# Optimization experiments

Hardware: AMD Instinct MI355X
Metric: run time of the kernel (lower is better)

## Reference

```python
import jax, jax.numpy as jnp
import numpy as np

B, H_, W_, C, HEADS, WS, SR = 4, 56, 56, 256, 8, 3, 4
HD = C // HEADS
N = H_ * W_
LL = WS * WS
PH, PW = H_ // SR, W_ // SR
PL = PH * PW
K_TAB = 2048


def _unfold3(x, H, W):
    # x: (B, C, H, W) -> (B, C, 9, H*W); matches torch nn.Unfold(kernel_size=3, padding=1)
    xp = jnp.pad(x, ((0, 0), (0, 0), (1, 1), (1, 1)))
    pats = jnp.stack([xp[:, :, i:i + H, j:j + W] for i in range(3) for j in range(3)], axis=2)
    return pats.reshape(x.shape[0], x.shape[1], 9, H * W)


def _l2n(x):
    # torch F.normalize(dim=-1) with eps=1e-12
    return x / jnp.maximum(jnp.linalg.norm(x, axis=-1, keepdims=True), 1e-12)


def setup_inputs() -> dict:
    key = jax.random.key(0)
    ks = jax.random.split(key, 24)
    x = jax.random.normal(ks[0], (B, N, C), jnp.float32)
    # padding mask from unfold of ones image (True where window element falls outside)
    ones = np.zeros((H_ + 2, W_ + 2), np.float32)
    ones[1:-1, 1:-1] = 1.0
    pats = np.stack([ones[i:i + H_, j:j + W_] for i in range(3) for j in range(3)], 0).reshape(9, N)
    padding_mask = jnp.asarray((pats == 0).T)  # (N, 9) bool
    local_valid = LL - padding_mask.sum(-1)
    seq_length_scale = jnp.log(local_valid.astype(jnp.float32) + PL)[:, None]  # (N,1)
    relative_pos_index = jax.random.randint(ks[1], (N * PL,), 0, K_TAB)
    relative_coords_table = jax.random.uniform(ks[2], (K_TAB, 2), jnp.float32, -1.0, 1.0)
    w = lambda k, shape: jax.random.normal(k, shape, jnp.float32) * 0.02
    inp = dict(
        x=x, H=H_, W=W_,
        relative_pos_index=relative_pos_index,
        relative_coords_table=relative_coords_table,
        seq_length_scale=seq_length_scale,
        padding_mask=padding_mask,
        q_w=w(ks[3], (C, C)), q_b=jnp.zeros((C,), jnp.float32),
        kv_w=w(ks[4], (2 * C, C)), kv_b=jnp.zeros((2 * C,), jnp.float32),
        sr_w=w(ks[5], (C, C)), sr_b=jnp.zeros((C,), jnp.float32),
        norm_g=jnp.ones((C,), jnp.float32), norm_b=jnp.zeros((C,), jnp.float32),
        cpb1_w=w(ks[6], (512, 2)), cpb1_b=jnp.zeros((512,), jnp.float32),
        cpb2_w=w(ks[7], (HEADS, 512)), cpb2_b=jnp.zeros((HEADS,), jnp.float32),
        temperature=jnp.log(jnp.exp(jnp.ones((HEADS, 1, 1), jnp.float32) / 0.24) - 1.0),
        query_embedding=w(ks[8], (HEADS, 1, HD)),
        rel_pos_bias_local=jax.random.normal(ks[9], (HEADS, LL), jnp.float32) * 0.0004,
        learnable_tokens=w(ks[10], (HEADS, HD, LL)),
        learnable_bias=jnp.zeros((HEADS, 1, LL), jnp.float32),
        proj_w=w(ks[11], (C, C)), proj_b=jnp.zeros((C,), jnp.float32),
    )
    return inp


def reference(x, H, W, relative_pos_index, relative_coords_table, seq_length_scale,
              padding_mask, q_w, q_b, kv_w, kv_b, sr_w, sr_b, norm_g, norm_b,
              cpb1_w, cpb1_b, cpb2_w, cpb2_b, temperature, query_embedding,
              rel_pos_bias_local, learnable_tokens, learnable_bias, proj_w, proj_b):
    Bsz, n, Cd = x.shape
    h, hd, ll = HEADS, HD, LL
    pH, pW = H // SR, W // SR
    pL = pH * pW
    # ----- queries -----
    q = (x @ q_w.T + q_b).reshape(Bsz, n, h, hd).transpose(0, 2, 1, 3)  # (B,h,N,d)
    q_norm = _l2n(q)
    q_scaled = (q_norm + query_embedding) * jax.nn.softplus(temperature) * seq_length_scale
    # ----- local branch: unfolded window KV -----
    kv = x @ kv_w.T + kv_b  # (B,N,2C)
    k_loc, v_loc = jnp.split(kv, 2, axis=-1)
    k_loc = _l2n(k_loc.reshape(Bsz, n, h, hd)).reshape(Bsz, n, Cd)
    kv_img = jnp.concatenate([k_loc, v_loc], -1).transpose(0, 2, 1).reshape(Bsz, 2 * Cd, H, W)
    pats = _unfold3(kv_img, H, W).reshape(Bsz, 2 * h, hd, ll, n).transpose(0, 1, 4, 2, 3)  # (B,2h,N,d,ll)
    k_local, v_local = jnp.split(pats, 2, axis=1)
    attn_local = jnp.einsum('bhnd,bhndl->bhnl', q_scaled, k_local) + rel_pos_bias_local[:, None, :]
    attn_local = jnp.where(padding_mask, -jnp.inf, attn_local)
    # ----- global branch: 1x1 conv -> GELU -> avg pool -> LN -> KV -----
    x_img = x.transpose(0, 2, 1).reshape(Bsz, Cd, H, W)
    x_sr = jax.nn.gelu(jnp.einsum('oc,bchw->bohw', sr_w, x_img) + sr_b[None, :, None, None], approximate=False)
    x_pool = x_sr.reshape(Bsz, Cd, pH, SR, pW, SR).mean(axis=(3, 5)).reshape(Bsz, Cd, pL).transpose(0, 2, 1)
    mu = x_pool.mean(-1, keepdims=True)
    var = x_pool.var(-1, keepdims=True)
    x_pool = (x_pool - mu) / jnp.sqrt(var + 1e-5) * norm_g + norm_b
    kvp = (x_pool @ kv_w.T + kv_b).reshape(Bsz, pL, 2 * h, hd).transpose(0, 2, 1, 3)
    k_pool, v_pool = jnp.split(kvp, 2, axis=1)  # each (B,h,pL,d)
    # CPB-MLP relative position bias (interpolate is identity since test==trained resolution)
    tab = jax.nn.relu(relative_coords_table @ cpb1_w.T + cpb1_b) @ cpb2_w.T + cpb2_b  # (K,h)
    pool_bias = tab.T[:, relative_pos_index].reshape(h, n, pL)
    attn_pool = jnp.einsum('bhnd,bhmd->bhnm', q_scaled, _l2n(k_pool)) + pool_bias
    # ----- joint softmax over [local | pool] -----
    attn = jax.nn.softmax(jnp.concatenate([attn_local, attn_pool], axis=-1), axis=-1)
    a_loc, a_pool = attn[..., :ll], attn[..., ll:]
    w_loc = jnp.einsum('bhnd,hdl->bhnl', q_norm, learnable_tokens) + learnable_bias + a_loc
    x_local = jnp.einsum('bhnl,bhndl->bhnd', w_loc, v_local)
    x_glob = jnp.einsum('bhnm,bhmd->bhnd', a_pool, v_pool)
    out = (x_local + x_glob).transpose(0, 2, 1, 3).reshape(Bsz, n, Cd)
    return out @ proj_w.T + proj_b
```

## Files before the change

kernel.cpp:

```cpp
#include <hip/hip_runtime.h>
#include <hip/hip_bf16.h>
#include <math.h>

#define Bn   4
#define Hh   56
#define Wn   56
#define Cn   256
#define NHn  8
#define HDn  32
#define Nn   3136
#define LLn  9
#define PLn  196
#define PWn  14
#define KTABn 2048
#define Mrows 12544
#define MP   224

#define XCNT   3211264
#define QWOFF  XCNT
#define KVWOFF (QWOFF + 65536)
#define SRWOFF (KVWOFF + 131072)
#define PWOFF  (SRWOFF + 65536)
#define TOTCVT (PWOFF + 65536)

typedef __attribute__((ext_vector_type(8))) short short8v;
typedef __attribute__((ext_vector_type(4))) float float4v;

__device__ __forceinline__ unsigned short f2b(float f) {
  __hip_bfloat16 h = __float2bfloat16(f);
  return *(unsigned short*)&h;
}
__device__ __forceinline__ float b2f(unsigned short u) {
  union { unsigned int i; float f; } x; x.i = ((unsigned int)u) << 16; return x.f;
}
__device__ __forceinline__ void u4_to8f(uint4 u, float* o) {
  o[0]=b2f((unsigned short)(u.x&0xffff)); o[1]=b2f((unsigned short)(u.x>>16));
  o[2]=b2f((unsigned short)(u.y&0xffff)); o[3]=b2f((unsigned short)(u.y>>16));
  o[4]=b2f((unsigned short)(u.z&0xffff)); o[5]=b2f((unsigned short)(u.z>>16));
  o[6]=b2f((unsigned short)(u.w&0xffff)); o[7]=b2f((unsigned short)(u.w>>16));
}

__launch_bounds__(256)
__global__ void cvt5(const float* __restrict__ x, const float* __restrict__ qw,
                     const float* __restrict__ kvw, const float* __restrict__ srw,
                     const float* __restrict__ pw, unsigned short* __restrict__ dst)
{
  const int i = (blockIdx.x * 256 + threadIdx.x) * 4;
  const float* src; int off;
  if      (i < XCNT)   { src = x;   off = 0; }
  else if (i < KVWOFF) { src = qw;  off = QWOFF; }
  else if (i < SRWOFF) { src = kvw; off = KVWOFF; }
  else if (i < PWOFF)  { src = srw; off = SRWOFF; }
  else                 { src = pw;  off = PWOFF; }
  const float4 v = *(const float4*)(src + (i - off));
  ushort4 o2;
  o2.x = f2b(v.x); o2.y = f2b(v.y); o2.z = f2b(v.z); o2.w = f2b(v.w);
  *(ushort4*)(dst + i) = o2;
}

template <int MODE>
__launch_bounds__(512)
__global__ void mgemm(const unsigned short* __restrict__ A,
                      const unsigned short* __restrict__ Wb,
                      const float* __restrict__ b0, const float* __restrict__ b1,
                      const float* __restrict__ b2, void* __restrict__ Cv, int Nc,
                      const float* __restrict__ sls, const float* __restrict__ qe,
                      const float* __restrict__ temp, float* __restrict__ Mq)
{
  __shared__ __align__(16) unsigned char smem[34816];
  unsigned short* As = (unsigned short*)smem;
  unsigned short* Bs = (unsigned short*)(smem + 16384);
  const int t = threadIdx.x;
  const int w = t >> 6, lane = t & 63;
  const int q = lane >> 4, ln = lane & 15;
  const int n0 = blockIdx.x * 128, m0 = blockIdx.y * 128;
  const int wm = (w >> 1) * 32, wn = (w & 1) * 64;

  float4v acc[2][4];
  #pragma unroll
  for (int mt = 0; mt < 2; ++mt)
    #pragma unroll
    for (int nt = 0; nt < 4; ++nt)
      acc[mt][nt] = (float4v){0.f, 0.f, 0.f, 0.f};

  for (int k0 = 0; k0 < 256; k0 += 64) {
    #pragma unroll
    for (int j = 0; j < 2; ++j) {
      const int u = t + 512 * j;
      const int r = u >> 3, cg = u & 7;
      const int cs = cg ^ (r & 7);
      const uint4 av = *(const uint4*)(A  + (size_t)(m0 + r) * 256 + k0 + cg * 8);
      *(uint4*)(As + r * 64 + cs * 8) = av;
      const uint4 bv = *(const uint4*)(Wb + (size_t)(n0 + r) * 256 + k0 + cg * 8);
      *(uint4*)(Bs + r * 64 + cs * 8) = bv;
    }
    __syncthreads();
    #pragma unroll
    for (int kk = 0; kk < 2; ++kk) {
      short8v af[2], bfr[4];
      const int cg = kk * 4 + q;
      #pragma unroll
      for (int mt = 0; mt < 2; ++mt) {
        const int r = wm + mt * 16 + ln;
        af[mt] = *(const short8v*)(As + r * 64 + (cg ^ (r & 7)) * 8);
      }
      #pragma unroll
      for (int nt = 0; nt < 4; ++nt) {
        const int r = wn + nt * 16 + ln;
        bfr[nt] = *(const short8v*)(Bs + r * 64 + (cg ^ (r & 7)) * 8);
      }
      #pragma unroll
      for (int mt = 0; mt < 2; ++mt)
        #pragma unroll
        for (int nt = 0; nt < 4; ++nt)
          acc[mt][nt] = __builtin_amdgcn_mfma_f32_16x16x32_bf16(af[mt], bfr[nt], acc[mt][nt], 0, 0, 0);
    }
    __syncthreads();
  }

  if constexpr (MODE == 0) {
    float* C = (float*)Cv;
    float* tileF = (float*)smem;
    float bia[4];
    #pragma unroll
    for (int nt = 0; nt < 4; ++nt) bia[nt] = b0[n0 + wn + nt * 16 + ln];
    #pragma unroll
    for (int half = 0; half < 2; ++half) {
      if ((w >> 2) == half) {
        #pragma unroll
        for (int mt = 0; mt < 2; ++mt)
          #pragma unroll
          for (int r = 0; r < 4; ++r)
            #pragma unroll
            for (int nt = 0; nt < 4; ++nt)
              tileF[(wm - half*64 + mt*16 + q*4 + r) * 132 + wn + nt*16 + ln] = acc[mt][nt][r] + bia[nt];
      }
      __syncthreads();
      #pragma unroll
      for (int j = 0; j < 4; ++j) {
        const int i = j * 512 + t;
        const int row = i >> 5, ch = i & 31;
        float4 v = *(const float4*)(tileF + row * 132 + ch * 4);
        *(float4*)(C + (size_t)(m0 + half * 64 + row) * Nc + n0 + ch * 4) = v;
      }
      __syncthreads();
    }
  } else {
    unsigned short* Cb = (unsigned short*)Cv;
    unsigned short* tileC = (unsigned short*)smem;
    const int seg = n0 >> 8;
    const int h0 = (n0 + wn) >> 5, h1 = h0 + 1;
    float spt0 = 0.f, spt1 = 0.f;
    if (seg == 0) { spt0 = log1pf(__expf(temp[h0])); spt1 = log1pf(__expf(temp[h1])); }
    float bia[4], qev[4];
    #pragma unroll
    for (int nt = 0; nt < 4; ++nt) {
      const int col = n0 + wn + nt * 16 + ln;
      bia[nt] = (seg == 0) ? b0[col] : (seg == 3 ? b2[col - 768] : b1[col - 256]);
      if (seg == 0) qev[nt] = qe[col];
    }
    #pragma unroll
    for (int mt = 0; mt < 2; ++mt) {
      #pragma unroll
      for (int r = 0; r < 4; ++r) {
        const int row = m0 + wm + mt * 16 + q * 4 + r;
        const int lrow = wm + mt * 16 + q * 4 + r;
        float vals[4];
        #pragma unroll
        for (int nt = 0; nt < 4; ++nt) vals[nt] = acc[mt][nt][r] + bia[nt];
        if (seg == 0) {
          float ss0 = vals[0]*vals[0] + vals[1]*vals[1];
          float ss1 = vals[2]*vals[2] + vals[3]*vals[3];
          #pragma unroll
          for (int mk = 1; mk <= 8; mk <<= 1) { ss0 += __shfl_xor(ss0, mk); ss1 += __shfl_xor(ss1, mk); }
          const float i0 = 1.f / fmaxf(sqrtf(ss0), 1e-12f);
          const float i1 = 1.f / fmaxf(sqrtf(ss1), 1e-12f);
          const int nidx = row % Nn, bb = row / Nn;
          const float sl = sls[nidx];
          float qsv[4];
          #pragma unroll
          for (int nt = 0; nt < 4; ++nt) {
            const float inv = (nt < 2) ? i0 : i1;
            const float sp  = (nt < 2) ? spt0 : spt1;
            qsv[nt] = (vals[nt] * inv + qev[nt]) * sp * sl;
          }
          float t0 = qsv[0]*qsv[0] + qsv[1]*qsv[1];
          float t1 = qsv[2]*qsv[2] + qsv[3]*qsv[3];
          #pragma unroll
          for (int mk = 1; mk <= 8; mk <<= 1) { t0 += __shfl_xor(t0, mk); t1 += __shfl_xor(t1, mk); }
          if (ln == 0) {
            Mq[((size_t)(bb * NHn + h0)) * Nn + nidx] = sqrtf(t0);
            Mq[((size_t)(bb * NHn + h1)) * Nn + nidx] = sqrtf(t1);
          }
          #pragma unroll
          for (int nt = 0; nt < 4; ++nt)
            tileC[lrow * 136 + wn + nt*16 + ln] = f2b(qsv[nt]);
        } else if (seg == 1) {
          float ss0 = vals[0]*vals[0] + vals[1]*vals[1];
          float ss1 = vals[2]*vals[2] + vals[3]*vals[3];
          #pragma unroll
          for (int mk = 1; mk <= 8; mk <<= 1) { ss0 += __shfl_xor(ss0, mk); ss1 += __shfl_xor(ss1, mk); }
          const float i0 = 1.f / fmaxf(sqrtf(ss0), 1e-12f);
          const float i1 = 1.f / fmaxf(sqrtf(ss1), 1e-12f);
          #pragma unroll
          for (int nt = 0; nt < 4; ++nt)
            tileC[lrow * 136 + wn + nt*16 + ln] = f2b(vals[nt] * ((nt < 2) ? i0 : i1));
        } else if (seg == 2) {
          #pragma unroll
          for (int nt = 0; nt < 4; ++nt)
            tileC[lrow * 136 + wn + nt*16 + ln] = f2b(vals[nt]);
        } else {
          #pragma unroll
          for (int nt = 0; nt < 4; ++nt) {
            const float v = vals[nt];
            tileC[lrow * 136 + wn + nt*16 + ln] =
              f2b(0.5f * v * (1.0f + erff(v * 0.70710678118654752f)));
          }
        }
      }
    }
    __syncthreads();
    #pragma unroll
    for (int j = 0; j < 4; ++j) {
      const int i = j * 512 + t;
      const int row = i >> 4, ch = i & 15;
      uint4 v = *(const uint4*)(tileC + row * 136 + ch * 8);
      *(uint4*)(Cb + (size_t)(m0 + row) * 1024 + n0 + ch * 8) = v;
    }
  }
}

__launch_bounds__(256)
__global__ void gemm_k(const float* __restrict__ A, const float* __restrict__ W,
                       const float* __restrict__ bias, float* __restrict__ Co,
                       int Mr, int Nc, int K)
{
  __shared__ __align__(16) float As[16][64];
  __shared__ __align__(16) float Ws[16][64];
  const int t  = threadIdx.x;
  const int m0 = blockIdx.y * 64, n0 = blockIdx.x * 64;
  const int lm = t >> 2, lk = (t & 3) << 2;
  const int tx = t & 15, ty = t >> 4;
  float acc[4][4] = {};
  int arow = m0 + lm; if (arow >= Mr) arow = Mr - 1;
  const int wrow = n0 + lm;
  for (int k0 = 0; k0 < K; k0 += 16) {
    float4 av = *(const float4*)(A + (size_t)arow * K + k0 + lk);
    As[lk+0][lm] = av.x; As[lk+1][lm] = av.y; As[lk+2][lm] = av.z; As[lk+3][lm] = av.w;
    float4 wv = *(const float4*)(W + (size_t)wrow * K + k0 + lk);
    Ws[lk+0][lm] = wv.x; Ws[lk+1][lm] = wv.y; Ws[lk+2][lm] = wv.z; Ws[lk+3][lm] = wv.w;
    __syncthreads();
    #pragma unroll
    for (int k = 0; k < 16; ++k) {
      float4 a = *(const float4*)&As[k][ty << 2];
      float4 w = *(const float4*)&Ws[k][tx << 2];
      acc[0][0] += a.x*w.x; acc[0][1] += a.x*w.y; acc[0][2] += a.x*w.z; acc[0][3] += a.x*w.w;
      acc[1][0] += a.y*w.x; acc[1][1] += a.y*w.y; acc[1][2] += a.y*w.z; acc[1][3] += a.y*w.w;
      acc[2][0] += a.z*w.x; acc[2][1] += a.z*w.y; acc[2][2] += a.z*w.z; acc[2][3] += a.z*w.w;
      acc[3][0] += a.w*w.x; acc[3][1] += a.w*w.y; acc[3][2] += a.w*w.z; acc[3][3] += a.w*w.w;
    }
    __syncthreads();
  }
  #pragma unroll
  for (int i = 0; i < 4; ++i) {
    const int row = m0 + (ty << 2) + i;
    if (row >= Mr) continue;
    #pragma unroll
    for (int j = 0; j < 4; ++j) {
      const int col = n0 + (tx << 2) + j;
      Co[(size_t)row * Nc + col] = acc[i][j] + bias[col];
    }
  }
}

__launch_bounds__(256)
__global__ void pool_ln_k(const unsigned short* __restrict__ fused, float* __restrict__ pln,
                          const float* __restrict__ g, const float* __restrict__ bb)
{
  const int blk = blockIdx.x;
  const int b = blk / PLn, pc = blk % PLn;
  const int pi = pc / PWn, pj = pc % PWn;
  const int c = threadIdx.x;
  float s = 0.f;
  #pragma unroll
  for (int r = 0; r < 4; ++r)
    #pragma unroll
    for (int cc = 0; cc < 4; ++cc) {
      const int n = (pi*4 + r) * Wn + pj*4 + cc;
      s += b2f(fused[((size_t)b * Nn + n) * 1024 + 768 + c]);
    }
  s *= (1.f/16.f);
  float sum = s, sq = s*s;
  #pragma unroll
  for (int m = 32; m >= 1; m >>= 1) { sum += __shfl_xor(sum, m); sq += __shfl_xor(sq, m); }
  __shared__ float sm[8];
  const int lane = c & 63, wid = c >> 6;
  if (lane == 0) { sm[wid] = sum; sm[4+wid] = sq; }
  __syncthreads();
  const float tot  = sm[0]+sm[1]+sm[2]+sm[3];
  const float totq = sm[4]+sm[5]+sm[6]+sm[7];
  const float mu  = tot * (1.f/256.f);
  const float var = totq * (1.f/256.f) - mu*mu;
  pln[(size_t)blk * Cn + c] = (s - mu) / sqrtf(var + 1e-5f) * g[c] + bb[c];
}

__launch_bounds__(256)
__global__ void pool_pack(const float* __restrict__ kvp, unsigned short* __restrict__ kbf,
                          unsigned short* __restrict__ vbf)
{
  const int bh = blockIdx.x;
  const int b = bh >> 3, h = bh & 7;
  const int t = threadIdx.x, mg = t >> 5, d = t & 31;
  for (int mi = 0; mi < MP/8; ++mi) {
    const int m = mi * 8 + mg;
    float kv2 = 0.f, vv = 0.f;
    if (m < PLn) {
      kv2 = kvp[((size_t)(b * PLn + m)) * 512 + h * HDn + d];
      vv  = kvp[((size_t)(b * PLn + m)) * 512 + 256 + h * HDn + d];
    }
    float ssn = kv2 * kv2;
    #pragma unroll
    for (int mm = 16; mm >= 1; mm >>= 1) ssn += __shfl_xor(ssn, mm);
    const float kn = (m < PLn) ? kv2 / fmaxf(sqrtf(ssn), 1e-12f) : 0.f;
    kbf[((size_t)bh * MP + m) * HDn + d] = f2b(kn);
    vbf[((size_t)bh * 33 + d) * MP + m] = f2b(vv);
  }
  for (int i = t; i < MP; i += 256)
    vbf[((size_t)bh * 33 + 32) * MP + i] = f2b(1.0f);
}

__launch_bounds__(64)
__global__ void cpb_k(const float* __restrict__ rct, const float* __restrict__ w1,
                      const float* __restrict__ b1, const float* __restrict__ w2,
                      const float* __restrict__ b2, float* __restrict__ tab)
{
  const int r = blockIdx.x, t = threadIdx.x;
  const float c0 = rct[r*2], c1 = rct[r*2+1];
  float part[8] = {};
  #pragma unroll
  for (int jj = 0; jj < 8; ++jj) {
    const int j = t * 8 + jj;
    float hv = fmaxf(c0 * w1[j*2] + c1 * w1[j*2+1] + b1[j], 0.f);
    #pragma unroll
    for (int h = 0; h < 8; ++h) part[h] += hv * w2[h*512 + j];
  }
  #pragma unroll
  for (int h = 0; h < 8; ++h)
    for (int mm = 32; mm >= 1; mm >>= 1) part[h] += __shfl_xor(part[h], mm);
  if (t < 8) tab[r*8 + t] = part[t] + b2[t];
}

__launch_bounds__(256)
__global__ void redmax_k(const float* __restrict__ tab, const float* __restrict__ rpb,
                         float* __restrict__ scal)
{
  float mx = -1e30f;
  for (int i = threadIdx.x; i < KTABn*NHn; i += 256) mx = fmaxf(mx, tab[i]);
  if (threadIdx.x < NHn*LLn) mx = fmaxf(mx, rpb[threadIdx.x]);
  #pragma unroll
  for (int m = 32; m >= 1; m >>= 1) mx = fmaxf(mx, __shfl_xor(mx, m));
  __shared__ float sm[4];
  if ((threadIdx.x & 63) == 0) sm[threadIdx.x >> 6] = mx;
  __syncthreads();
  if (threadIdx.x == 0) scal[0] = fmaxf(fmaxf(sm[0], sm[1]), fmaxf(sm[2], sm[3]));
}

__launch_bounds__(256)
__global__ void bias_g2(const int* __restrict__ rpi, const float* __restrict__ tab,
                        unsigned short* __restrict__ bias2)
{
  const int tid = blockIdx.x * 256 + threadIdx.x;
  const int n = tid / MP, m = tid - n * MP;
  if (m < PLn) {
    const int idx = rpi[(size_t)n * PLn + m];
    #pragma unroll
    for (int h = 0; h < NHn; ++h)
      bias2[((size_t)h * Nn + n) * MP + m] = f2b(tab[(size_t)idx * NHn + h]);
  } else {
    #pragma unroll
    for (int h = 0; h < NHn; ++h)
      bias2[((size_t)h * Nn + n) * MP + m] = 0xFF80;
  }
}

__launch_bounds__(256)
__global__ void attn_f(const unsigned short* __restrict__ fused,
                       const unsigned short* __restrict__ kbf,
                       const unsigned short* __restrict__ vbf,
                       const unsigned short* __restrict__ bias2,
                       const float* __restrict__ Mq, const float* __restrict__ scal,
                       const float* __restrict__ slsp, const float* __restrict__ temp,
                       const float* __restrict__ qe, const float* __restrict__ lt,
                       const float* __restrict__ lb, const float* __restrict__ rpb,
                       unsigned short* __restrict__ outp)
{
  __shared__ __align__(16) unsigned short sh[32256];
  unsigned short* k_lds = sh;
  unsigned short* v_lds = sh + 7168;
  unsigned short* p_lds = sh + 17920;
  float* tabf = (float*)(v_lds + 33 * MP);
  float* qe_s  = tabf;
  float* lt_s  = tabf + 32;
  float* lb_s  = tabf + 320;
  float* rpb_s = tabf + 329;
  const int t = threadIdx.x;
  const int w = t >> 6, lane = t & 63;
  const int ln = lane & 15, quad = lane >> 4;
  const int tile = blockIdx.x, h = blockIdx.y, b = blockIdx.z;
  const int bh = b * NHn + h;

  {
    const uint4* gk = (const uint4*)(kbf + (size_t)bh * (MP * HDn));
    uint4* lk = (uint4*)k_lds;
    for (int i = t; i < 896; i += 256) lk[i] = gk[i];
    const uint4* gv = (const uint4*)(vbf + (size_t)bh * (33 * MP));
    uint4* lv = (uint4*)v_lds;
    for (int i = t; i < 924; i += 256) lv[i] = gv[i];
    if (t < 32) qe_s[t] = qe[h * HDn + t];
    for (int i = t; i < HDn * LLn; i += 256) lt_s[i] = lt[h * HDn * LLn + i];
    if (t < LLn) { lb_s[t] = lb[h * LLn + t]; rpb_s[t] = rpb[h * LLn + t]; }
  }
  __syncthreads();

  const int nb = tile * 64 + w * 16;
  const short8v afrag = *(const short8v*)(fused +
      ((size_t)(b * Nn + nb + ln)) * 1024 + h * HDn + quad * 8);
  float M4[4];
  const float sc = scal[0];
  #pragma unroll
  for (int r = 0; r < 4; ++r) M4[r] = Mq[(size_t)bh * Nn + nb + quad * 4 + r] + sc;

  unsigned short* pst = p_lds + w * (16 * MP);
  #pragma unroll
  for (int mt = 0; mt < 14; ++mt) {
    short8v bfrag = *(const short8v*)(k_lds + (mt * 16 + ln) * HDn + quad * 8);
    float4v s = __builtin_amdgcn_mfma_f32_16x16x32_bf16(afrag, bfrag,
                                                        (float4v){0.f,0.f,0.f,0.f}, 0, 0, 0);
    #pragma unroll
    for (int r = 0; r < 4; ++r) {
      const int nr = nb + quad * 4 + r;
      const float bv = b2f(bias2[((size_t)h * Nn + nr) * MP + mt * 16 + ln]);
      const float p = __expf(s[r] + bv - M4[r]);
      pst[(quad * 4 + r) * MP + mt * 16 + ln] = f2b(p);
    }
  }

  float4v accO[3];
  accO[0] = (float4v){0.f,0.f,0.f,0.f};
  accO[1] = (float4v){0.f,0.f,0.f,0.f};
  accO[2] = (float4v){0.f,0.f,0.f,0.f};
  #pragma unroll
  for (int kc = 0; kc < 7; ++kc) {
    short8v pa = *(const short8v*)(pst + ln * MP + kc * 32 + quad * 8);
    #pragma unroll
    for (int nt = 0; nt < 3; ++nt) {
      short8v vb = *(const short8v*)(v_lds + (nt * 16 + ln) * MP + kc * 32 + quad * 8);
      accO[nt] = __builtin_amdgcn_mfma_f32_16x16x32_bf16(pa, vb, accO[nt], 0, 0, 0);
    }
  }
  float* pool_w = (float*)pst;
  #pragma unroll
  for (int r = 0; r < 4; ++r) {
    const int row = quad * 4 + r;
    pool_w[row * 33 + ln]      = accO[0][r];
    pool_w[row * 33 + 16 + ln] = accO[1][r];
    if (ln == 0) pool_w[row * 33 + 32] = accO[2][r];
  }

  const int nl = t >> 2, dg = t & 3;
  const int n = tile * 64 + nl;
  const unsigned short* qp = fused + ((size_t)(b * Nn + n)) * 1024 + h * HDn + dg * 8;
  float qs8[8];
  u4_to8f(*(const uint4*)qp, qs8);
  const float M = Mq[(size_t)bh * Nn + n] + sc;
  const float spt = log1pf(__expf(temp[h]));
  const float inv_qs = 1.f / (spt * slsp[n]);

  float acc8[8], ext8[8];
  #pragma unroll
  for (int j = 0; j < 8; ++j) { acc8[j] = 0.f; ext8[j] = 0.f; }
  float l_run = 0.f;
  const int pi = n / Wn, pj = n % Wn;
  #pragma unroll
  for (int lc = 0; lc < LLn; ++lc) {
    const int ii = pi + lc/3 - 1, jj = pj + (lc%3) - 1;
    if (ii < 0 || ii >= Hh || jj < 0 || jj >= Wn) continue;
    const int nb2 = ii * Wn + jj;
    const unsigned short* kr = fused + ((size_t)(b * Nn + nb2)) * 1024 + 256 + h * HDn + dg * 8;
    float kk8[8], vv8[8];
    u4_to8f(*(const uint4*)kr, kk8);
    u4_to8f(*(const uint4*)(kr + 256), vv8);
    float pp = 0.f, ep = 0.f;
    #pragma unroll
    for (int j = 0; j < 8; ++j) {
      pp += qs8[j] * kk8[j];
      ep += (qs8[j] * inv_qs - qe_s[dg*8 + j]) * lt_s[(dg*8 + j) * LLn + lc];
    }
    pp += __shfl_xor(pp, 1); pp += __shfl_xor(pp, 2);
    ep += __shfl_xor(ep, 1); ep += __shfl_xor(ep, 2);
    const float e = ep + lb_s[lc];
    const float p = __expf(pp + rpb_s[lc] - M);
    l_run += p;
    #pragma unroll
    for (int j = 0; j < 8; ++j) { acc8[j] += p * vv8[j]; ext8[j] += e * vv8[j]; }
  }

  const float* pool_r = (float*)(p_lds + w * (16 * MP)) + (nl - w * 16) * 33;
  const float l_pool = pool_r[32];
  const float invl = 1.f / (l_run + l_pool);
  uint4 u;
  {
    const float* op = pool_r + dg * 8;
    float o0 = (acc8[0]+op[0])*invl + ext8[0], o1 = (acc8[1]+op[1])*invl + ext8[1];
    float o2 = (acc8[2]+op[2])*invl + ext8[2], o3 = (acc8[3]+op[3])*invl + ext8[3];
    float o4 = (acc8[4]+op[4])*invl + ext8[4], o5 = (acc8[5]+op[5])*invl + ext8[5];
    float o6 = (acc8[6]+op[6])*invl + ext8[6], o7 = (acc8[7]+op[7])*invl + ext8[7];
    u.x = f2b(o0) | ((unsigned int)f2b(o1) << 16);
    u.y = f2b(o2) | ((unsigned int)f2b(o3) << 16);
    u.z = f2b(o4) | ((unsigned int)f2b(o5) << 16);
    u.w = f2b(o6) | ((unsigned int)f2b(o7) << 16);
  }
  *(uint4*)(outp + ((size_t)b * Nn + n) * Cn + h * HDn + dg * 8) = u;
}

extern "C" void kernel_launch(void* const* d_in, const int* in_sizes, int n_in,
                              void* d_out, int out_size, void* d_ws, size_t ws_size,
                              hipStream_t stream)
{
  const float* x    = (const float*)d_in[0];
  const int*   rpi  = (const int*)d_in[3];
  const float* rct  = (const float*)d_in[4];
  const float* sls  = (const float*)d_in[5];
  const float* q_w  = (const float*)d_in[7];
  const float* q_b  = (const float*)d_in[8];
  const float* kv_w = (const float*)d_in[9];
  const float* kv_b = (const float*)d_in[10];
  const float* sr_w = (const float*)d_in[11];
  const float* sr_b = (const float*)d_in[12];
  const float* ng   = (const float*)d_in[13];
  const float* nbta = (const float*)d_in[14];
  const float* c1w  = (const float*)d_in[15];
  const float* c1b  = (const float*)d_in[16];
  const float* c2w  = (const float*)d_in[17];
  const float* c2b  = (const float*)d_in[18];
  const float* temp = (const float*)d_in[19];
  const float* qe   = (const float*)d_in[20];
  const float* rpb  = (const float*)d_in[21];
  const float* lt   = (const float*)d_in[22];
  const float* lb   = (const float*)d_in[23];
  const float* pw   = (const float*)d_in[24];
  const float* pb   = (const float*)d_in[25];

  float* ws = (float*)d_ws;
  size_t o = 0;
  unsigned short* bf = (unsigned short*)(ws + o); o += TOTCVT / 2;
  unsigned short* fused = (unsigned short*)(ws + o); o += (size_t)Mrows * 512;
  float* Mq    = ws + o;  o += (size_t)Bn * NHn * Nn;
  float* pln   = ws + o;  o += (size_t)Bn * PLn * Cn;
  float* kvp   = ws + o;  o += (size_t)Bn * PLn * 2 * Cn;
  unsigned short* kbf = (unsigned short*)(ws + o); o += (size_t)Bn * NHn * MP * HDn / 2;
  unsigned short* vbf = (unsigned short*)(ws + o); o += (size_t)Bn * NHn * 33 * MP / 2;
  float* tab   = ws + o;  o += (size_t)KTABn * NHn;
  float* scal  = ws + o;  o += 8;
  unsigned short* bias2 = (unsigned short*)(ws + o); o += (size_t)NHn * Nn * MP / 2;
  unsigned short* outp  = (unsigned short*)(ws + o); o += (size_t)Mrows * Cn / 2;

  const unsigned short* xbf   = bf;
  const unsigned short* qkvsw = bf + QWOFF;
  const unsigned short* pwbf  = bf + PWOFF;

  cvt5<<<TOTCVT/1024, 256, 0, stream>>>(x, q_w, kv_w, sr_w, pw, bf);
  mgemm<1><<<dim3(8, 98), 512, 0, stream>>>(xbf, qkvsw, q_b, kv_b, sr_b, fused, 1024,
                                            sls, qe, temp, Mq);
  pool_ln_k<<<Bn*PLn, 256, 0, stream>>>(fused, pln, ng, nbta);
  gemm_k<<<dim3(8, 13), 256, 0, stream>>>(pln, kv_w, kv_b, kvp, Bn*PLn, 512, 256);
  pool_pack<<<Bn*NHn, 256, 0, stream>>>(kvp, kbf, vbf);
  cpb_k<<<KTABn, 64, 0, stream>>>(rct, c1w, c1b, c2w, c2b, tab);
  redmax_k<<<1, 256, 0, stream>>>(tab, rpb, scal);
  bias_g2<<<(Nn*MP)/256, 256, 0, stream>>>(rpi, tab, bias2);
  attn_f<<<dim3(49, NHn, Bn), 256, 0, stream>>>(fused, kbf, vbf, bias2, Mq, scal,
                                                sls, temp, qe, lt, lb, rpb, outp);
  mgemm<0><<<dim3(2, 98), 512, 0, stream>>>(outp, pwbf, pb, pb, pb, (float*)d_out, 256,
                                            nullptr, nullptr, nullptr, nullptr);
}
```

Before: 259.6 us.

## Stream pooled K/V from global memory and interleave QK and PV per chunk

The attention kernel no longer stages the per-head pooled K and V tiles in shared memory. It reads MFMA fragments straight from global/L2 and interleaves the score/exp step with the P·V accumulation in 32-column chunks. The softmax denominator is now summed in registers with lane shuffles rather than computed by an extra all-ones row of V, so the pack kernel writes 32 V rows instead of 33. Shared memory drops from about 63 KB to about 15 KB, which should raise occupancy and remove the bulk LDS fill and its barrier, at the cost of uncoalesced, repeated global fragment loads served by cache.

```diff
diff --git a/kernel.cpp b/kernel.cpp
--- a/kernel.cpp
+++ b/kernel.cpp
@@ -323,10 +323,8 @@
     for (int mm = 16; mm >= 1; mm >>= 1) ssn += __shfl_xor(ssn, mm);
     const float kn = (m < PLn) ? kv2 / fmaxf(sqrtf(ssn), 1e-12f) : 0.f;
     kbf[((size_t)bh * MP + m) * HDn + d] = f2b(kn);
-    vbf[((size_t)bh * 33 + d) * MP + m] = f2b(vv);
-  }
-  for (int i = t; i < MP; i += 256)
-    vbf[((size_t)bh * 33 + 32) * MP + i] = f2b(1.0f);
+    vbf[((size_t)bh * 32 + d) * MP + m] = f2b(vv);
+  }
 }
 
 __launch_bounds__(64)
@@ -394,11 +392,10 @@
                        const float* __restrict__ lb, const float* __restrict__ rpb,
                        unsigned short* __restrict__ outp)
 {
-  __shared__ __align__(16) unsigned short sh[32256];
-  unsigned short* k_lds = sh;
-  unsigned short* v_lds = sh + 7168;
-  unsigned short* p_lds = sh + 17920;
-  float* tabf = (float*)(v_lds + 33 * MP);
+  __shared__ __align__(16) unsigned short sh[7488];
+  unsigned short* p_lds = sh;
+  float* park = (float*)(sh + 2560);
+  float* tabf = park + 2112;
   float* qe_s  = tabf;
   float* lt_s  = tabf + 32;
   float* lb_s  = tabf + 320;
@@ -409,17 +406,9 @@
   const int tile = blockIdx.x, h = blockIdx.y, b = blockIdx.z;
   const int bh = b * NHn + h;
 
-  {
-    const uint4* gk = (const uint4*)(kbf + (size_t)bh * (MP * HDn));
-    uint4* lk = (uint4*)k_lds;
-    for (int i = t; i < 896; i += 256) lk[i] = gk[i];
-    const uint4* gv = (const uint4*)(vbf + (size_t)bh * (33 * MP));
-    uint4* lv = (uint4*)v_lds;
-    for (int i = t; i < 924; i += 256) lv[i] = gv[i];
-    if (t < 32) qe_s[t] = qe[h * HDn + t];
-    for (int i = t; i < HDn * LLn; i += 256) lt_s[i] = lt[h * HDn * LLn + i];
-    if (t < LLn) { lb_s[t] = lb[h * LLn + t]; rpb_s[t] = rpb[h * LLn + t]; }
-  }
+  if (t < 32) qe_s[t] = qe[h * HDn + t];
+  for (int i = t; i < HDn * LLn; i += 256) lt_s[i] = lt[h * HDn * LLn + i];
+  if (t < LLn) { lb_s[t] = lb[h * LLn + t]; rpb_s[t] = rpb[h * LLn + t]; }
   __syncthreads();
 
   const int nb = tile * 64 + w * 16;
@@ -430,41 +419,54 @@
   #pragma unroll
   for (int r = 0; r < 4; ++r) M4[r] = Mq[(size_t)bh * Nn + nb + quad * 4 + r] + sc;
 
-  unsigned short* pst = p_lds + w * (16 * MP);
-  #pragma unroll
-  for (int mt = 0; mt < 14; ++mt) {
-    short8v bfrag = *(const short8v*)(k_lds + (mt * 16 + ln) * HDn + quad * 8);
-    float4v s = __builtin_amdgcn_mfma_f32_16x16x32_bf16(afrag, bfrag,
-                                                        (float4v){0.f,0.f,0.f,0.f}, 0, 0, 0);
-    #pragma unroll
-    for (int r = 0; r < 4; ++r) {
-      const int nr = nb + quad * 4 + r;
-      const float bv = b2f(bias2[((size_t)h * Nn + nr) * MP + mt * 16 + ln]);
-      const float p = __expf(s[r] + bv - M4[r]);
-      pst[(quad * 4 + r) * MP + mt * 16 + ln] = f2b(p);
-    }
-  }
-
-  float4v accO[3];
+  const unsigned short* kg = kbf + (size_t)bh * (MP * HDn);
+  const unsigned short* vg = vbf + (size_t)bh * (32 * MP);
+  unsigned short* pst = p_lds + w * 640;
+
+  float4v accO[2];
   accO[0] = (float4v){0.f,0.f,0.f,0.f};
   accO[1] = (float4v){0.f,0.f,0.f,0.f};
-  accO[2] = (float4v){0.f,0.f,0.f,0.f};
+  float lsum[4] = {0.f, 0.f, 0.f, 0.f};
+
   #pragma unroll
   for (int kc = 0; kc < 7; ++kc) {
-    short8v pa = *(const short8v*)(pst + ln * MP + kc * 32 + quad * 8);
-    #pragma unroll
-    for (int nt = 0; nt < 3; ++nt) {
-      short8v vb = *(const short8v*)(v_lds + (nt * 16 + ln) * MP + kc * 32 + quad * 8);
+    #pragma unroll
+    for (int mtl = 0; mtl < 2; ++mtl) {
+      const int mt = kc * 2 + mtl;
+      short8v bfrag = *(const short8v*)(kg + (mt * 16 + ln) * HDn + quad * 8);
+      float4v s = __builtin_amdgcn_mfma_f32_16x16x32_bf16(afrag, bfrag,
+                                                          (float4v){0.f,0.f,0.f,0.f}, 0, 0, 0);
+      #pragma unroll
+      for (int r = 0; r < 4; ++r) {
+        const int nr = nb + quad * 4 + r;
+        const float bv = b2f(bias2[((size_t)h * Nn + nr) * MP + mt * 16 + ln]);
+        const float p = __expf(s[r] + bv - M4[r]);
+        const unsigned short pb = f2b(p);
+        lsum[r] += b2f(pb);
+        pst[(quad * 4 + r) * 40 + mtl * 16 + ln] = pb;
+      }
+    }
+    short8v pa = *(const short8v*)(pst + ln * 40 + quad * 8);
+    #pragma unroll
+    for (int nt = 0; nt < 2; ++nt) {
+      short8v vb = *(const short8v*)(vg + (size_t)(nt * 16 + ln) * MP + kc * 32 + quad * 8);
       accO[nt] = __builtin_amdgcn_mfma_f32_16x16x32_bf16(pa, vb, accO[nt], 0, 0, 0);
     }
   }
-  float* pool_w = (float*)pst;
+
+  #pragma unroll
+  for (int r = 0; r < 4; ++r) {
+    #pragma unroll
+    for (int mk = 1; mk <= 8; mk <<= 1) lsum[r] += __shfl_xor(lsum[r], mk);
+  }
+
+  float* mypark = park + w * 528;
   #pragma unroll
   for (int r = 0; r < 4; ++r) {
     const int row = quad * 4 + r;
-    pool_w[row * 33 + ln]      = accO[0][r];
-    pool_w[row * 33 + 16 + ln] = accO[1][r];
-    if (ln == 0) pool_w[row * 33 + 32] = accO[2][r];
+    mypark[row * 33 + ln]      = accO[0][r];
+    mypark[row * 33 + 16 + ln] = accO[1][r];
+    if (ln == 0) mypark[row * 33 + 32] = lsum[r];
   }
 
   const int nl = t >> 2, dg = t & 3;
@@ -505,7 +507,7 @@
     for (int j = 0; j < 8; ++j) { acc8[j] += p * vv8[j]; ext8[j] += e * vv8[j]; }
   }
 
-  const float* pool_r = (float*)(p_lds + w * (16 * MP)) + (nl - w * 16) * 33;
+  const float* pool_r = park + w * 528 + (nl - w * 16) * 33;
   const float l_pool = pool_r[32];
   const float invl = 1.f / (l_run + l_pool);
   uint4 u;
@@ -559,7 +561,7 @@
   float* pln   = ws + o;  o += (size_t)Bn * PLn * Cn;
   float* kvp   = ws + o;  o += (size_t)Bn * PLn * 2 * Cn;
   unsigned short* kbf = (unsigned short*)(ws + o); o += (size_t)Bn * NHn * MP * HDn / 2;
-  unsigned short* vbf = (unsigned short*)(ws + o); o += (size_t)Bn * NHn * 33 * MP / 2;
+  unsigned short* vbf = (unsigned short*)(ws + o); o += (size_t)Bn * NHn * 32 * MP / 2;
   float* tab   = ws + o;  o += (size_t)KTABn * NHn;
   float* scal  = ws + o;  o += 8;
   unsigned short* bias2 = (unsigned short*)(ws + o); o += (size_t)NHn * Nn * MP / 2;
```

Result: faster. 251.7 us (-3.0%).
